# Kernel optimization log

Measured on AMD Instinct MI355X. Metric: run time of the kernel, lower is better.

## Reference

```python
import jax, jax.numpy as jnp
import numpy as np

N = 50000      # nodes
E = 1_600_000  # edges
D = 512        # input_dim == embedding_dim (see notes: fc_emb output is dead code)
H = 256        # hidden_channels
G = 16         # graphs in the batch


def setup_inputs() -> dict:
    key = jax.random.key(0)
    ks = jax.random.split(key, 16)
    x = jax.random.normal(ks[0], (N, D), dtype=jnp.float32)
    edge_index = jax.random.randint(ks[1], (2, E), 0, N, dtype=jnp.int64)
    batch = jnp.sort(jax.random.randint(ks[2], (N,), 0, G, dtype=jnp.int64))

    def lin(k, fi, fo):
        s = 1.0 / np.sqrt(fi)
        return jax.random.uniform(k, (fi, fo), jnp.float32, -s, s)

    return {
        "x": x,
        "edge_index": edge_index,
        "batch": batch,
        "W1": lin(ks[3], D, H), "b1": jnp.zeros((H,), jnp.float32),
        "W2": lin(ks[4], H, H), "b2": jnp.zeros((H,), jnp.float32),
        "W3": lin(ks[5], H, H), "b3": jnp.zeros((H,), jnp.float32),
        "Wf": lin(ks[6], H, 64), "bf": jnp.zeros((64,), jnp.float32),
        "Wp": lin(ks[7], 64, 1), "bp": jnp.zeros((1,), jnp.float32),
    }


def _gcn_conv(h, src, dst, norm, W, b):
    # GCNConv: out[i] = sum_{j->i} norm_ji * (h[j] @ W) + b  (self-loops included in src/dst)
    m = h @ W                                    # [N, out]  transform first (smaller gather)
    agg = jax.ops.segment_sum(m[src] * norm[:, None], dst, num_segments=N)
    return agg + b


def reference(x, edge_index, batch, W1, b1, W2, b2, W3, b3, Wf, bf, Wp, bp):
    loops = jnp.arange(N, dtype=edge_index.dtype)
    src = jnp.concatenate([edge_index[0], loops])   # [E+N]
    dst = jnp.concatenate([edge_index[1], loops])
    # symmetric normalization D^{-1/2} (A+I) D^{-1/2}; degree over targets incl. self-loops
    deg = jax.ops.segment_sum(jnp.ones_like(dst, jnp.float32), dst, num_segments=N)
    dinv = jnp.where(deg > 0, jax.lax.rsqrt(deg), 0.0)
    norm = dinv[src] * dinv[dst]                    # [E+N]

    h = jax.nn.relu(_gcn_conv(x, src, dst, norm, W1, b1))
    h = jax.nn.relu(_gcn_conv(h, src, dst, norm, W2, b2))
    h = _gcn_conv(h, src, dst, norm, W3, b3)

    # global_mean_pool over graph ids
    counts = jax.ops.segment_sum(jnp.ones((N,), jnp.float32), batch, num_segments=G)
    pooled = jax.ops.segment_sum(h, batch, num_segments=G) / jnp.maximum(counts, 1.0)[:, None]

    # dropout treated as identity (eval-mode determinism for baseline)
    out = pooled @ Wf + bf
    out = out @ Wp + bp
    return jax.nn.sigmoid(out)
```

## Files before the change

kernel.cpp:

```cpp
#include <hip/hip_runtime.h>
#include <hip/hip_bf16.h>

#define NN 50000
#define EE 1600000
#define DD 512
#define HH 256
#define GG 16
#define BK 96
#define NCH 256
#define CHSZ 6250

typedef long fp8x8;
typedef __attribute__((ext_vector_type(4))) float f32x4;
typedef __attribute__((ext_vector_type(2))) float f32x2;

__device__ __forceinline__ unsigned char f2fp8(float f) {
    return (unsigned char)(__builtin_amdgcn_cvt_pk_fp8_f32(f, f, 0, false) & 0xff);
}
__device__ __forceinline__ unsigned int pk4fp8(float a, float b, float c, float d) {
    unsigned int r = __builtin_amdgcn_cvt_pk_fp8_f32(a, b, 0, false);
    return __builtin_amdgcn_cvt_pk_fp8_f32(c, d, r, true);
}

__global__ __launch_bounds__(256) void k_hist_cvt(const int* __restrict__ ei,
                                                  unsigned int* __restrict__ histg,
                                                  const float* __restrict__ x, unsigned char* __restrict__ xb,
                                                  const float* __restrict__ W1, const float* __restrict__ W2,
                                                  const float* __restrict__ W3, unsigned char* __restrict__ W1t,
                                                  unsigned char* __restrict__ W2t, unsigned char* __restrict__ W3t) {
    __shared__ unsigned int hp[6250];
    int b = blockIdx.x, t = threadIdx.x;
    if (b < 1024) {
        int j = b >> 2, q = b & 3;
        int dlo = q * 12500;
        for (int i = t; i < 6250; i += 256) hp[i] = 0;
        __syncthreads();
        int base = j * CHSZ;
        for (int k = 0; k < 25; ++k) {
            int o = k * 256 + t;
            if (o < CHSZ) {
                int d = ei[EE + base + o];
                unsigned int ld = (unsigned)(d - dlo);
                if (ld < 12500u) atomicAdd(&hp[ld >> 1], (ld & 1) ? 65536u : 1u);
            }
        }
        __syncthreads();
        unsigned int* dst = histg + j * 25000 + q * 6250;
        for (int i = t; i < 6250; i += 256) dst[i] = hp[i];
    } else if (b < 7274) {
        size_t i0 = ((size_t)(b - 1024) * 256 + t) * 16;
        float4 v0 = *(const float4*)(x + i0);
        float4 v1 = *(const float4*)(x + i0 + 4);
        float4 v2 = *(const float4*)(x + i0 + 8);
        float4 v3 = *(const float4*)(x + i0 + 12);
        uint4 o;
        o.x = pk4fp8(v0.x, v0.y, v0.z, v0.w);
        o.y = pk4fp8(v1.x, v1.y, v1.z, v1.w);
        o.z = pk4fp8(v2.x, v2.y, v2.z, v2.w);
        o.w = pk4fp8(v3.x, v3.y, v3.z, v3.w);
        *(uint4*)(xb + i0) = o;
    } else {
        int u = (b - 7274) * 256 + t;
        if (u < 131072) {
            int k = u >> 8, n = u & 255;
            W1t[(size_t)n * 512 + k] = f2fp8(W1[u]);
        } else if (u < 196608) {
            int q = u - 131072; int k = q >> 8, n = q & 255;
            W2t[(size_t)n * 256 + k] = f2fp8(W2[q]);
        } else {
            int q = u - 196608; int k = q >> 8, n = q & 255;
            W3t[(size_t)n * 256 + k] = f2fp8(W3[q]);
        }
    }
}

__global__ __launch_bounds__(256) void k_scan(const unsigned int* __restrict__ histg,
                                              unsigned int* __restrict__ offg,
                                              int* __restrict__ cnt, float* __restrict__ dinv) {
    __shared__ unsigned int part[8][32];
    int t = threadIdx.x;
    int il = t & 31, g = t >> 5;
    int i = blockIdx.x * 32 + il;
    bool ok = (i < 25000);
    unsigned int hv[32];
    unsigned int p0 = 0, p1 = 0;
    if (ok) {
        const unsigned int* hp = histg + (size_t)(g * 32) * 25000 + i;
        #pragma unroll
        for (int jj = 0; jj < 32; ++jj) hv[jj] = hp[(size_t)jj * 25000];
        #pragma unroll
        for (int jj = 0; jj < 32; ++jj) { p0 += hv[jj] & 0xffffu; p1 += hv[jj] >> 16; }
    }
    part[g][il] = p0 | (p1 << 16);
    __syncthreads();
    unsigned int b0 = 0, b1 = 0;
    #pragma unroll
    for (int g2 = 0; g2 < 7; ++g2) {
        if (g2 < g) { unsigned int p = part[g2][il]; b0 += p & 0xffffu; b1 += p >> 16; }
    }
    if (ok && g == 7) {
        unsigned int tot0 = b0 + p0, tot1 = b1 + p1;
        cnt[2 * i]     = (int)tot0;
        cnt[2 * i + 1] = (int)tot1;
        dinv[2 * i]     = rsqrtf((float)tot0 + 1.0f);
        dinv[2 * i + 1] = rsqrtf((float)tot1 + 1.0f);
    }
    if (ok) {
        unsigned int run0 = b0, run1 = b1;
        unsigned int* op = offg + (size_t)(g * 32) * 25000 + i;
        #pragma unroll
        for (int jj = 0; jj < 32; ++jj) {
            op[(size_t)jj * 25000] = run0 | (run1 << 16);
            run0 += hv[jj] & 0xffffu; run1 += hv[jj] >> 16;
        }
    }
}

__global__ __launch_bounds__(256) void k_place(const int* __restrict__ ei,
                                               const unsigned int* __restrict__ offg,
                                               unsigned short* __restrict__ bucket) {
    __shared__ unsigned int cur[3125];
    int b = blockIdx.x, t = threadIdx.x;
    int x8 = b & 7, j = b >> 3;
    int lo = x8 * CHSZ;
    for (int i = t; i < 3125; i += 256) cur[i] = 0;
    __syncthreads();
    int base = j * CHSZ;
    for (int k = 0; k < 25; ++k) {
        int o = k * 256 + t;
        if (o < CHSZ) {
            int d = ei[EE + base + o];
            unsigned ld = (unsigned)(d - lo);
            if (ld < 6250u) {
                int s = ei[base + o];
                unsigned old = atomicAdd(&cur[ld >> 1], (ld & 1) ? 65536u : 1u);
                unsigned rank = (ld & 1) ? (old >> 16) : (old & 0xffffu);
                unsigned ov = offg[j * 25000 + (d >> 1)];
                unsigned pos = ((d & 1) ? (ov >> 16) : (ov & 0xffffu)) + rank;
                if (pos < BK) bucket[(size_t)d * BK + pos] = (unsigned short)s;
            }
        }
    }
}

__global__ __launch_bounds__(256) void k_gemm_fp8(const unsigned char* __restrict__ A,
                                                  const unsigned char* __restrict__ Bt,
                                                  const float* __restrict__ dinv,
                                                  unsigned char* __restrict__ C, int M, int K) {
    __shared__ unsigned char As[2][8192];
    __shared__ unsigned char Bs[2][8192];
    const int tid  = threadIdx.x;
    const int wave = tid >> 6;
    const int lane = tid & 63;
    const int row0 = blockIdx.x * 128;
    const int col0 = blockIdx.y * 128;
    const int wr = wave & 1;
    const int wc = wave >> 1;
    const int l15 = lane & 15;
    const int quad = lane >> 4;

    const int srow = (wave << 4) + (lane >> 2);
    const int gk16 = (((lane & 3) ^ (srow & 3)) << 4);
    int arow1 = row0 + srow;      if (arow1 >= M) arow1 = M - 1;
    int arow2 = row0 + srow + 64; if (arow2 >= M) arow2 = M - 1;
    const int brow1 = col0 + srow;
    const int brow2 = brow1 + 64;

#define STAGE(BUF, KB) do {                                                              \
    const unsigned char* ga1_ = A  + (size_t)arow1 * K + (KB) + gk16;                    \
    const unsigned char* ga2_ = A  + (size_t)arow2 * K + (KB) + gk16;                    \
    const unsigned char* gb1_ = Bt + (size_t)brow1 * K + (KB) + gk16;                    \
    const unsigned char* gb2_ = Bt + (size_t)brow2 * K + (KB) + gk16;                    \
    __builtin_amdgcn_global_load_lds((const __attribute__((address_space(1))) void*)ga1_,\
        (__attribute__((address_space(3))) void*)&As[BUF][wave * 1024], 16, 0, 0);       \
    __builtin_amdgcn_global_load_lds((const __attribute__((address_space(1))) void*)ga2_,\
        (__attribute__((address_space(3))) void*)&As[BUF][4096 + wave * 1024], 16, 0, 0);\
    __builtin_amdgcn_global_load_lds((const __attribute__((address_space(1))) void*)gb1_,\
        (__attribute__((address_space(3))) void*)&Bs[BUF][wave * 1024], 16, 0, 0);       \
    __builtin_amdgcn_global_load_lds((const __attribute__((address_space(1))) void*)gb2_,\
        (__attribute__((address_space(3))) void*)&Bs[BUF][4096 + wave * 1024], 16, 0, 0);\
} while (0)

    f32x4 acc[4][4];
    #pragma unroll
    for (int i = 0; i < 4; ++i)
        #pragma unroll
        for (int j = 0; j < 4; ++j)
            acc[i][j] = (f32x4){0.f, 0.f, 0.f, 0.f};

    const int NT = K >> 6;
    STAGE(0, 0);
    __syncthreads();

    for (int t = 0; t < NT; ++t) {
        const int cb = t & 1;
        if (t + 1 < NT) STAGE(cb ^ 1, (t + 1) << 6);

        fp8x8 af[2][4], bfr[2][4];
        #pragma unroll
        for (int kk = 0; kk < 2; ++kk) {
            const int csw = (((kk * 2 + (quad >> 1)) ^ (l15 & 3)) << 4) + ((quad & 1) << 3);
            #pragma unroll
            for (int mi = 0; mi < 4; ++mi) {
                af[kk][mi]  = *(const fp8x8*)&As[cb][(wr * 64 + mi * 16 + l15) * 64 + csw];
                bfr[kk][mi] = *(const fp8x8*)&Bs[cb][(wc * 64 + mi * 16 + l15) * 64 + csw];
            }
        }
        #pragma unroll
        for (int kk = 0; kk < 2; ++kk)
            #pragma unroll
            for (int mi = 0; mi < 4; ++mi)
                #pragma unroll
                for (int ni = 0; ni < 4; ++ni)
                    acc[mi][ni] = __builtin_amdgcn_mfma_f32_16x16x32_fp8_fp8(af[kk][mi], bfr[kk][ni], acc[mi][ni], 0, 0, 0);

        __syncthreads();
    }
#undef STAGE

    #pragma unroll
    for (int mi = 0; mi < 4; ++mi) {
        #pragma unroll
        for (int r = 0; r < 4; ++r) {
            int grow = row0 + wr * 64 + mi * 16 + quad * 4 + r;
            if (grow < M) {
                float ds = dinv[grow];
                #pragma unroll
                for (int ni = 0; ni < 4; ++ni) {
                    int gcol = col0 + wc * 64 + ni * 16 + l15;
                    C[(size_t)grow * 256 + gcol] = f2fp8(ds * acc[mi][ni][r]);
                }
            }
        }
    }
}

__global__ __launch_bounds__(256) void k_agg(const unsigned int* __restrict__ m,
                                             const float* __restrict__ bias,
                                             const float* __restrict__ dinv, const int* __restrict__ cnt,
                                             const unsigned short* __restrict__ bucket,
                                             unsigned int* __restrict__ outb,
                                             int do_relu) {
    int lane = threadIdx.x & 63;
    int node = blockIdx.x * 4 + (threadIdx.x >> 6);
    if (node >= NN) return;
    const unsigned int* mrow = m + lane;
    unsigned int v = mrow[(size_t)node * 64];
    f32x2 lo = __builtin_amdgcn_cvt_pk_f32_fp8(v, false);
    f32x2 hi = __builtin_amdgcn_cvt_pk_f32_fp8(v, true);
    float4 acc = make_float4(lo.x, lo.y, hi.x, hi.y);
    int n = cnt[node]; if (n > BK) n = BK;
    const unsigned short* cs = bucket + (size_t)node * BK;
    int p = 0;
    for (; p + 16 <= n; p += 16) {
        uint4 iv0 = *(const uint4*)(cs + p);
        uint4 iv1 = *(const uint4*)(cs + p + 8);
        unsigned int u0 = mrow[(size_t)(iv0.x & 0xffffu) * 64];
        unsigned int u1 = mrow[(size_t)(iv0.x >> 16)    * 64];
        unsigned int u2 = mrow[(size_t)(iv0.y & 0xffffu) * 64];
        unsigned int u3 = mrow[(size_t)(iv0.y >> 16)    * 64];
        unsigned int u4 = mrow[(size_t)(iv0.z & 0xffffu) * 64];
        unsigned int u5 = mrow[(size_t)(iv0.z >> 16)    * 64];
        unsigned int u6 = mrow[(size_t)(iv0.w & 0xffffu) * 64];
        unsigned int u7 = mrow[(size_t)(iv0.w >> 16)    * 64];
        unsigned int u8 = mrow[(size_t)(iv1.x & 0xffffu) * 64];
        unsigned int u9 = mrow[(size_t)(iv1.x >> 16)    * 64];
        unsigned int ua = mrow[(size_t)(iv1.y & 0xffffu) * 64];
        unsigned int ub = mrow[(size_t)(iv1.y >> 16)    * 64];
        unsigned int uc = mrow[(size_t)(iv1.z & 0xffffu) * 64];
        unsigned int ud = mrow[(size_t)(iv1.z >> 16)    * 64];
        unsigned int ue = mrow[(size_t)(iv1.w & 0xffffu) * 64];
        unsigned int uf = mrow[(size_t)(iv1.w >> 16)    * 64];
        f32x2 a0 = __builtin_amdgcn_cvt_pk_f32_fp8(u0, false), b0 = __builtin_amdgcn_cvt_pk_f32_fp8(u0, true);
        f32x2 a1 = __builtin_amdgcn_cvt_pk_f32_fp8(u1, false), b1 = __builtin_amdgcn_cvt_pk_f32_fp8(u1, true);
        f32x2 a2 = __builtin_amdgcn_cvt_pk_f32_fp8(u2, false), b2 = __builtin_amdgcn_cvt_pk_f32_fp8(u2, true);
        f32x2 a3 = __builtin_amdgcn_cvt_pk_f32_fp8(u3, false), b3 = __builtin_amdgcn_cvt_pk_f32_fp8(u3, true);
        f32x2 a4 = __builtin_amdgcn_cvt_pk_f32_fp8(u4, false), b4 = __builtin_amdgcn_cvt_pk_f32_fp8(u4, true);
        f32x2 a5 = __builtin_amdgcn_cvt_pk_f32_fp8(u5, false), b5 = __builtin_amdgcn_cvt_pk_f32_fp8(u5, true);
        f32x2 a6 = __builtin_amdgcn_cvt_pk_f32_fp8(u6, false), b6 = __builtin_amdgcn_cvt_pk_f32_fp8(u6, true);
        f32x2 a7 = __builtin_amdgcn_cvt_pk_f32_fp8(u7, false), b7 = __builtin_amdgcn_cvt_pk_f32_fp8(u7, true);
        f32x2 a8 = __builtin_amdgcn_cvt_pk_f32_fp8(u8, false), b8 = __builtin_amdgcn_cvt_pk_f32_fp8(u8, true);
        f32x2 a9 = __builtin_amdgcn_cvt_pk_f32_fp8(u9, false), b9 = __builtin_amdgcn_cvt_pk_f32_fp8(u9, true);
        f32x2 aa = __builtin_amdgcn_cvt_pk_f32_fp8(ua, false), ba = __builtin_amdgcn_cvt_pk_f32_fp8(ua, true);
        f32x2 ab = __builtin_amdgcn_cvt_pk_f32_fp8(ub, false), bb2 = __builtin_amdgcn_cvt_pk_f32_fp8(ub, true);
        f32x2 ac = __builtin_amdgcn_cvt_pk_f32_fp8(uc, false), bc = __builtin_amdgcn_cvt_pk_f32_fp8(uc, true);
        f32x2 ad = __builtin_amdgcn_cvt_pk_f32_fp8(ud, false), bd = __builtin_amdgcn_cvt_pk_f32_fp8(ud, true);
        f32x2 ae = __builtin_amdgcn_cvt_pk_f32_fp8(ue, false), be = __builtin_amdgcn_cvt_pk_f32_fp8(ue, true);
        f32x2 af2 = __builtin_amdgcn_cvt_pk_f32_fp8(uf, false), bf2 = __builtin_amdgcn_cvt_pk_f32_fp8(uf, true);
        acc.x += (((a0.x + a1.x) + (a2.x + a3.x)) + ((a4.x + a5.x) + (a6.x + a7.x)))
               + (((a8.x + a9.x) + (aa.x + ab.x)) + ((ac.x + ad.x) + (ae.x + af2.x)));
        acc.y += (((a0.y + a1.y) + (a2.y + a3.y)) + ((a4.y + a5.y) + (a6.y + a7.y)))
               + (((a8.y + a9.y) + (aa.y + ab.y)) + ((ac.y + ad.y) + (ae.y + af2.y)));
        acc.z += (((b0.x + b1.x) + (b2.x + b3.x)) + ((b4.x + b5.x) + (b6.x + b7.x)))
               + (((b8.x + b9.x) + (ba.x + bb2.x)) + ((bc.x + bd.x) + (be.x + bf2.x)));
        acc.w += (((b0.y + b1.y) + (b2.y + b3.y)) + ((b4.y + b5.y) + (b6.y + b7.y)))
               + (((b8.y + b9.y) + (ba.y + bb2.y)) + ((bc.y + bd.y) + (be.y + bf2.y)));
    }
    for (; p + 8 <= n; p += 8) {
        uint4 iv0 = *(const uint4*)(cs + p);
        unsigned int u0 = mrow[(size_t)(iv0.x & 0xffffu) * 64];
        unsigned int u1 = mrow[(size_t)(iv0.x >> 16)    * 64];
        unsigned int u2 = mrow[(size_t)(iv0.y & 0xffffu) * 64];
        unsigned int u3 = mrow[(size_t)(iv0.y >> 16)    * 64];
        unsigned int u4 = mrow[(size_t)(iv0.z & 0xffffu) * 64];
        unsigned int u5 = mrow[(size_t)(iv0.z >> 16)    * 64];
        unsigned int u6 = mrow[(size_t)(iv0.w & 0xffffu) * 64];
        unsigned int u7 = mrow[(size_t)(iv0.w >> 16)    * 64];
        f32x2 a0 = __builtin_amdgcn_cvt_pk_f32_fp8(u0, false), b0 = __builtin_amdgcn_cvt_pk_f32_fp8(u0, true);
        f32x2 a1 = __builtin_amdgcn_cvt_pk_f32_fp8(u1, false), b1 = __builtin_amdgcn_cvt_pk_f32_fp8(u1, true);
        f32x2 a2 = __builtin_amdgcn_cvt_pk_f32_fp8(u2, false), b2 = __builtin_amdgcn_cvt_pk_f32_fp8(u2, true);
        f32x2 a3 = __builtin_amdgcn_cvt_pk_f32_fp8(u3, false), b3 = __builtin_amdgcn_cvt_pk_f32_fp8(u3, true);
        f32x2 a4 = __builtin_amdgcn_cvt_pk_f32_fp8(u4, false), b4 = __builtin_amdgcn_cvt_pk_f32_fp8(u4, true);
        f32x2 a5 = __builtin_amdgcn_cvt_pk_f32_fp8(u5, false), b5 = __builtin_amdgcn_cvt_pk_f32_fp8(u5, true);
        f32x2 a6 = __builtin_amdgcn_cvt_pk_f32_fp8(u6, false), b6 = __builtin_amdgcn_cvt_pk_f32_fp8(u6, true);
        f32x2 a7 = __builtin_amdgcn_cvt_pk_f32_fp8(u7, false), b7 = __builtin_amdgcn_cvt_pk_f32_fp8(u7, true);
        acc.x += ((a0.x + a1.x) + (a2.x + a3.x)) + ((a4.x + a5.x) + (a6.x + a7.x));
        acc.y += ((a0.y + a1.y) + (a2.y + a3.y)) + ((a4.y + a5.y) + (a6.y + a7.y));
        acc.z += ((b0.x + b1.x) + (b2.x + b3.x)) + ((b4.x + b5.x) + (b6.x + b7.x));
        acc.w += ((b0.y + b1.y) + (b2.y + b3.y)) + ((b4.y + b5.y) + (b6.y + b7.y));
    }
    for (; p < n; ++p) {
        int s = cs[p];
        unsigned int u = mrow[(size_t)s * 64];
        f32x2 a = __builtin_amdgcn_cvt_pk_f32_fp8(u, false);
        f32x2 b = __builtin_amdgcn_cvt_pk_f32_fp8(u, true);
        acc.x += a.x; acc.y += a.y; acc.z += b.x; acc.w += b.y;
    }
    float di = dinv[node];
    const float4 bb = *(const float4*)(bias + lane * 4);
    acc.x = acc.x * di + bb.x; acc.y = acc.y * di + bb.y;
    acc.z = acc.z * di + bb.z; acc.w = acc.w * di + bb.w;
    if (do_relu) {
        acc.x = fmaxf(acc.x, 0.f); acc.y = fmaxf(acc.y, 0.f);
        acc.z = fmaxf(acc.z, 0.f); acc.w = fmaxf(acc.w, 0.f);
    }
    outb[(size_t)node * 64 + lane] = pk4fp8(acc.x, acc.y, acc.z, acc.w);
}

__global__ __launch_bounds__(256) void k_pool(const unsigned int* __restrict__ h,
                                              const int* __restrict__ batch,
                                              float* __restrict__ pooled, float* __restrict__ cnts) {
    __shared__ float pl[GG * 256];
    __shared__ float cl[GG];
    int t = threadIdx.x;
    for (int i = t; i < GG * 256; i += 256) pl[i] = 0.f;
    if (t < GG) cl[t] = 0.f;
    __syncthreads();
    int sub = t >> 6;
    int fd = t & 63;
    int chunk = (NN + gridDim.x - 1) / gridDim.x;
    int i0 = blockIdx.x * chunk;
    int i1 = i0 + chunk; if (i1 > NN) i1 = NN;
    int gcur = -1;
    float a0 = 0.f, a1 = 0.f, a2 = 0.f, a3 = 0.f, cr = 0.f;
    for (int i = i0 + sub; i < i1; i += 4) {
        int g = batch[i];
        if (g != gcur) {
            if (gcur >= 0) {
                atomicAdd(&pl[gcur * 256 + fd * 4 + 0], a0);
                atomicAdd(&pl[gcur * 256 + fd * 4 + 1], a1);
                atomicAdd(&pl[gcur * 256 + fd * 4 + 2], a2);
                atomicAdd(&pl[gcur * 256 + fd * 4 + 3], a3);
                if (fd == 0) atomicAdd(&cl[gcur], cr);
            }
            gcur = g; a0 = a1 = a2 = a3 = 0.f; cr = 0.f;
        }
        unsigned int u = h[(size_t)i * 64 + fd];
        f32x2 lo = __builtin_amdgcn_cvt_pk_f32_fp8(u, false);
        f32x2 hi = __builtin_amdgcn_cvt_pk_f32_fp8(u, true);
        a0 += lo.x; a1 += lo.y; a2 += hi.x; a3 += hi.y;
        cr += 1.f;
    }
    if (gcur >= 0) {
        atomicAdd(&pl[gcur * 256 + fd * 4 + 0], a0);
        atomicAdd(&pl[gcur * 256 + fd * 4 + 1], a1);
        atomicAdd(&pl[gcur * 256 + fd * 4 + 2], a2);
        atomicAdd(&pl[gcur * 256 + fd * 4 + 3], a3);
        if (fd == 0) atomicAdd(&cl[gcur], cr);
    }
    __syncthreads();
    for (int i = t; i < GG * 256; i += 256)
        if (pl[i] != 0.f) atomicAdd(&pooled[i], pl[i]);
    if (t < GG && cl[t] != 0.f) atomicAdd(&cnts[t], cl[t]);
}

__global__ __launch_bounds__(1024) void k_head(const float* __restrict__ pooled, const float* __restrict__ cnts,
                                               const float* __restrict__ Wf, const float* __restrict__ bf,
                                               const float* __restrict__ Wp, const float* __restrict__ bp,
                                               float* __restrict__ out) {
    __shared__ float z[GG][64];
    int t = threadIdx.x;
    int g = t >> 6, j = t & 63;
    float inv = 1.f / fmaxf(cnts[g], 1.f);
    float acc = 0.f;
    for (int k = 0; k < 256; ++k) acc += pooled[g * 256 + k] * Wf[k * 64 + j];
    z[g][j] = acc * inv + bf[j];
    __syncthreads();
    if (t < GG) {
        float o = 0.f;
        for (int j2 = 0; j2 < 64; ++j2) o += z[t][j2] * Wp[j2];
        o += bp[0];
        out[t] = 1.f / (1.f + expf(-o));
    }
}

extern "C" void kernel_launch(void* const* d_in, const int* in_sizes, int n_in,
                              void* d_out, int out_size, void* d_ws, size_t ws_size,
                              hipStream_t stream) {
    const float* x   = (const float*)d_in[0];
    const int*   ei  = (const int*)d_in[1];
    const int*   bat = (const int*)d_in[2];
    const float* W1  = (const float*)d_in[3];
    const float* b1  = (const float*)d_in[4];
    const float* W2  = (const float*)d_in[5];
    const float* b2  = (const float*)d_in[6];
    const float* W3  = (const float*)d_in[7];
    const float* b3  = (const float*)d_in[8];
    const float* Wf  = (const float*)d_in[9];
    const float* bf  = (const float*)d_in[10];
    const float* Wp  = (const float*)d_in[11];
    const float* bp  = (const float*)d_in[12];
    float* out = (float*)d_out;

    char* w = (char*)d_ws;
    unsigned char* xb  = (unsigned char*)w;  w += (size_t)NN * DD;
    unsigned char* mb  = (unsigned char*)w;  w += (size_t)NN * HH;
    unsigned char* hb  = (unsigned char*)w;  w += (size_t)NCH * 25000 * 4;
    unsigned char* hb2 = (unsigned char*)w;  w += (size_t)NCH * 25000 * 4;
    unsigned char* W1t = (unsigned char*)w;  w += (size_t)DD * HH;
    unsigned char* W2t = (unsigned char*)w;  w += (size_t)HH * HH;
    unsigned char* W3t = (unsigned char*)w;  w += (size_t)HH * HH;
    float* dinv   = (float*)w;               w += (size_t)NN * 4;
    int*   cnt    = (int*)w;                 w += (size_t)NN * 4;
    unsigned short* bucket = (unsigned short*)w; w += (size_t)NN * BK * 2;
    float* pooled = (float*)w;               w += (size_t)GG * HH * 4;
    float* cnts   = (float*)w;               w += (size_t)GG * 4;

    unsigned int* histg = (unsigned int*)hb;
    unsigned int* offg  = (unsigned int*)hb2;

    hipMemsetAsync(pooled, 0, (size_t)(GG * HH + GG) * 4, stream);

    k_hist_cvt<<<8298, 256, 0, stream>>>(ei, histg, x, xb, W1, W2, W3, W1t, W2t, W3t);
    k_scan<<<782, 256, 0, stream>>>(histg, offg, cnt, dinv);
    k_place<<<2048, 256, 0, stream>>>(ei, offg, bucket);

    dim3 gg((NN + 127) / 128, 2);
    k_gemm_fp8<<<gg, 256, 0, stream>>>(xb, W1t, dinv, mb, NN, DD);
    k_agg<<<(NN + 3) / 4, 256, 0, stream>>>((const unsigned int*)mb, b1, dinv, cnt, bucket,
                                            (unsigned int*)hb, 1);
    k_gemm_fp8<<<gg, 256, 0, stream>>>(hb, W2t, dinv, mb, NN, HH);
    k_agg<<<(NN + 3) / 4, 256, 0, stream>>>((const unsigned int*)mb, b2, dinv, cnt, bucket,
                                            (unsigned int*)hb2, 1);
    k_gemm_fp8<<<gg, 256, 0, stream>>>(hb2, W3t, dinv, mb, NN, HH);
    k_agg<<<(NN + 3) / 4, 256, 0, stream>>>((const unsigned int*)mb, b3, dinv, cnt, bucket,
                                            (unsigned int*)hb, 0);

    k_pool<<<256, 256, 0, stream>>>((const unsigned int*)hb, bat, pooled, cnts);
    k_head<<<1, 1024, 0, stream>>>(pooled, cnts, Wf, bf, Wp, bp, out);
}
```

Measured before the change: 518.5 us.

## Pack histogram to 8-bit counters, sort neighbor lists by source, fuse pool with head

Measured after the change: 545.8 us. +5.3%, slower.

```diff
diff --git a/kernel.cpp b/kernel.cpp
--- a/kernel.cpp
+++ b/kernel.cpp
@@ -30,9 +30,9 @@
                                                   unsigned char* __restrict__ W2t, unsigned char* __restrict__ W3t) {
     __shared__ unsigned int hp[6250];
     int b = blockIdx.x, t = threadIdx.x;
-    if (b < 1024) {
-        int j = b >> 2, q = b & 3;
-        int dlo = q * 12500;
+    if (b < 512) {
+        int j = b >> 1, half = b & 1;
+        int dlo = half * 25000;
         for (int i = t; i < 6250; i += 256) hp[i] = 0;
         __syncthreads();
         int base = j * CHSZ;
@@ -41,14 +41,14 @@
             if (o < CHSZ) {
                 int d = ei[EE + base + o];
                 unsigned int ld = (unsigned)(d - dlo);
-                if (ld < 12500u) atomicAdd(&hp[ld >> 1], (ld & 1) ? 65536u : 1u);
+                if (ld < 25000u) atomicAdd(&hp[ld >> 2], 1u << ((ld & 3) * 8));
             }
         }
         __syncthreads();
-        unsigned int* dst = histg + j * 25000 + q * 6250;
+        unsigned int* dst = histg + (size_t)j * 12500 + half * 6250;
         for (int i = t; i < 6250; i += 256) dst[i] = hp[i];
-    } else if (b < 7274) {
-        size_t i0 = ((size_t)(b - 1024) * 256 + t) * 16;
+    } else if (b < 6762) {
+        size_t i0 = ((size_t)(b - 512) * 256 + t) * 16;
         float4 v0 = *(const float4*)(x + i0);
         float4 v1 = *(const float4*)(x + i0 + 4);
         float4 v2 = *(const float4*)(x + i0 + 8);
@@ -60,7 +60,7 @@
         o.w = pk4fp8(v3.x, v3.y, v3.z, v3.w);
         *(uint4*)(xb + i0) = o;
     } else {
-        int u = (b - 7274) * 256 + t;
+        int u = (b - 6762) * 256 + t;
         if (u < 131072) {
             int k = u >> 8, n = u & 255;
             W1t[(size_t)n * 512 + k] = f2fp8(W1[u]);
@@ -76,42 +76,50 @@
 
 __global__ __launch_bounds__(256) void k_scan(const unsigned int* __restrict__ histg,
                                               unsigned int* __restrict__ offg,
-                                              int* __restrict__ cnt, float* __restrict__ dinv) {
-    __shared__ unsigned int part[8][32];
-    int t = threadIdx.x;
-    int il = t & 31, g = t >> 5;
-    int i = blockIdx.x * 32 + il;
-    bool ok = (i < 25000);
-    unsigned int hv[32];
-    unsigned int p0 = 0, p1 = 0;
+                                              int* __restrict__ cnt, float* __restrict__ dinv,
+                                              unsigned int* __restrict__ zero0) {
+    __shared__ unsigned int part[512];
+    int t = threadIdx.x, b = blockIdx.x;
+    if (b == 391) {
+        for (int i = t; i < GG * 256 + GG + 1; i += 256) zero0[i] = 0u;
+        return;
+    }
+    const int il = t & 31, g = t >> 5;
+    const int g4 = b * 32 + il;
+    const bool ok = (g4 < 12500);
+    unsigned hv[32];
+    unsigned s02 = 0, s13 = 0;
     if (ok) {
-        const unsigned int* hp = histg + (size_t)(g * 32) * 25000 + i;
-        #pragma unroll
-        for (int jj = 0; jj < 32; ++jj) hv[jj] = hp[(size_t)jj * 25000];
-        #pragma unroll
-        for (int jj = 0; jj < 32; ++jj) { p0 += hv[jj] & 0xffffu; p1 += hv[jj] >> 16; }
-    }
-    part[g][il] = p0 | (p1 << 16);
-    __syncthreads();
-    unsigned int b0 = 0, b1 = 0;
+        const unsigned* hp = histg + (size_t)(g * 32) * 12500 + g4;
+        #pragma unroll
+        for (int jj = 0; jj < 32; ++jj) hv[jj] = hp[(size_t)jj * 12500];
+        #pragma unroll
+        for (int jj = 0; jj < 32; ++jj) { s02 += hv[jj] & 0x00ff00ffu; s13 += (hv[jj] >> 8) & 0x00ff00ffu; }
+    }
+    part[t * 2] = s02; part[t * 2 + 1] = s13;
+    __syncthreads();
+    unsigned b02 = 0, b13 = 0;
     #pragma unroll
-    for (int g2 = 0; g2 < 7; ++g2) {
-        if (g2 < g) { unsigned int p = part[g2][il]; b0 += p & 0xffffu; b1 += p >> 16; }
-    }
+    for (int g2 = 0; g2 < 7; ++g2)
+        if (g2 < g) { b02 += part[(g2 * 32 + il) * 2]; b13 += part[(g2 * 32 + il) * 2 + 1]; }
     if (ok && g == 7) {
-        unsigned int tot0 = b0 + p0, tot1 = b1 + p1;
-        cnt[2 * i]     = (int)tot0;
-        cnt[2 * i + 1] = (int)tot1;
-        dinv[2 * i]     = rsqrtf((float)tot0 + 1.0f);
-        dinv[2 * i + 1] = rsqrtf((float)tot1 + 1.0f);
+        unsigned t02 = b02 + s02, t13 = b13 + s13;
+        int4 cv; cv.x = (int)(t02 & 0xffffu); cv.y = (int)(t13 & 0xffffu);
+        cv.z = (int)(t02 >> 16);      cv.w = (int)(t13 >> 16);
+        *(int4*)(cnt + 4 * g4) = cv;
+        float4 dv;
+        dv.x = rsqrtf((float)cv.x + 1.0f); dv.y = rsqrtf((float)cv.y + 1.0f);
+        dv.z = rsqrtf((float)cv.z + 1.0f); dv.w = rsqrtf((float)cv.w + 1.0f);
+        *(float4*)(dinv + 4 * g4) = dv;
     }
     if (ok) {
-        unsigned int run0 = b0, run1 = b1;
-        unsigned int* op = offg + (size_t)(g * 32) * 25000 + i;
+        unsigned r0 = b02 & 0xffffu, r2 = b02 >> 16, r1 = b13 & 0xffffu, r3 = b13 >> 16;
         #pragma unroll
         for (int jj = 0; jj < 32; ++jj) {
-            op[(size_t)jj * 25000] = run0 | (run1 << 16);
-            run0 += hv[jj] & 0xffffu; run1 += hv[jj] >> 16;
+            uint2 wv; wv.x = r0 | (r1 << 16); wv.y = r2 | (r3 << 16);
+            *(uint2*)(offg + (size_t)(g * 32 + jj) * 25000 + 2 * g4) = wv;
+            unsigned h = hv[jj];
+            r0 += h & 0xffu; r1 += (h >> 8) & 0xffu; r2 += (h >> 16) & 0xffu; r3 += h >> 24;
         }
     }
 }
@@ -140,6 +148,33 @@
                 if (pos < BK) bucket[(size_t)d * BK + pos] = (unsigned short)s;
             }
         }
+    }
+}
+
+__global__ __launch_bounds__(256) void k_sort(const int* __restrict__ cnt,
+                                              const unsigned short* __restrict__ bucket,
+                                              unsigned short* __restrict__ bucket2) {
+    __shared__ unsigned int binc[4][16], rk[4][16];
+    int w = threadIdx.x >> 6, l = threadIdx.x & 63;
+    int node = blockIdx.x * 4 + w;
+    if (l < 16) { binc[w][l] = 0; rk[w][l] = 0; }
+    __syncthreads();
+    int n = cnt[node]; if (n > BK) n = BK;
+    const unsigned short* cs = bucket + (size_t)node * BK;
+    unsigned s0 = 0, s1 = 0; int b0 = -1, b1 = -1;
+    if (l < n)      { s0 = cs[l];      b0 = (int)(s0 >> 12); atomicAdd(&binc[w][b0], 1u); }
+    if (l + 64 < n) { s1 = cs[l + 64]; b1 = (int)(s1 >> 12); atomicAdd(&binc[w][b1], 1u); }
+    __syncthreads();
+    unsigned short* ds = bucket2 + (size_t)node * BK;
+    if (b0 >= 0) {
+        unsigned base = 0;
+        for (int q = 0; q < b0; ++q) base += binc[w][q];
+        ds[base + atomicAdd(&rk[w][b0], 1u)] = (unsigned short)s0;
+    }
+    if (b1 >= 0) {
+        unsigned base = 0;
+        for (int q = 0; q < b1; ++q) base += binc[w][q];
+        ds[base + atomicAdd(&rk[w][b1], 1u)] = (unsigned short)s1;
     }
 }
 
@@ -337,11 +372,17 @@
     outb[(size_t)node * 64 + lane] = pk4fp8(acc.x, acc.y, acc.z, acc.w);
 }
 
-__global__ __launch_bounds__(256) void k_pool(const unsigned int* __restrict__ h,
-                                              const int* __restrict__ batch,
-                                              float* __restrict__ pooled, float* __restrict__ cnts) {
+__global__ __launch_bounds__(256) void k_poolhead(const unsigned int* __restrict__ h,
+                                                  const int* __restrict__ batch,
+                                                  float* __restrict__ pooled, float* __restrict__ cnts,
+                                                  unsigned int* __restrict__ ctr,
+                                                  const float* __restrict__ Wf, const float* __restrict__ bf,
+                                                  const float* __restrict__ Wp, const float* __restrict__ bp,
+                                                  float* __restrict__ out) {
     __shared__ float pl[GG * 256];
     __shared__ float cl[GG];
+    __shared__ float z[GG][64];
+    __shared__ unsigned int lastdone;
     int t = threadIdx.x;
     for (int i = t; i < GG * 256; i += 256) pl[i] = 0.f;
     if (t < GG) cl[t] = 0.f;
@@ -382,19 +423,25 @@
     for (int i = t; i < GG * 256; i += 256)
         if (pl[i] != 0.f) atomicAdd(&pooled[i], pl[i]);
     if (t < GG && cl[t] != 0.f) atomicAdd(&cnts[t], cl[t]);
-}
-
-__global__ __launch_bounds__(1024) void k_head(const float* __restrict__ pooled, const float* __restrict__ cnts,
-                                               const float* __restrict__ Wf, const float* __restrict__ bf,
-                                               const float* __restrict__ Wp, const float* __restrict__ bp,
-                                               float* __restrict__ out) {
-    __shared__ float z[GG][64];
-    int t = threadIdx.x;
-    int g = t >> 6, j = t & 63;
-    float inv = 1.f / fmaxf(cnts[g], 1.f);
-    float acc = 0.f;
-    for (int k = 0; k < 256; ++k) acc += pooled[g * 256 + k] * Wf[k * 64 + j];
-    z[g][j] = acc * inv + bf[j];
+
+    __syncthreads();
+    __threadfence();
+    if (t == 0) lastdone = (atomicAdd(ctr, 1u) == gridDim.x - 1) ? 1u : 0u;
+    __syncthreads();
+    if (!lastdone) return;
+    __threadfence();
+    for (int i = t; i < GG * 256; i += 256)
+        pl[i] = __hip_atomic_load(&pooled[i], __ATOMIC_RELAXED, __HIP_MEMORY_SCOPE_AGENT);
+    if (t < GG)
+        cl[t] = __hip_atomic_load(&cnts[t], __ATOMIC_RELAXED, __HIP_MEMORY_SCOPE_AGENT);
+    __syncthreads();
+    for (int idx = t; idx < GG * 64; idx += 256) {
+        int g = idx >> 6, j = idx & 63;
+        float inv = 1.f / fmaxf(cl[g], 1.f);
+        float acc = 0.f;
+        for (int k = 0; k < 256; ++k) acc += pl[g * 256 + k] * Wf[k * 64 + j];
+        z[g][j] = acc * inv + bf[j];
+    }
     __syncthreads();
     if (t < GG) {
         float o = 0.f;
@@ -432,30 +479,31 @@
     unsigned char* W3t = (unsigned char*)w;  w += (size_t)HH * HH;
     float* dinv   = (float*)w;               w += (size_t)NN * 4;
     int*   cnt    = (int*)w;                 w += (size_t)NN * 4;
-    unsigned short* bucket = (unsigned short*)w; w += (size_t)NN * BK * 2;
+    unsigned short* bucket  = (unsigned short*)w; w += (size_t)NN * BK * 2;
+    unsigned short* bucket2 = (unsigned short*)w; w += (size_t)NN * BK * 2;
     float* pooled = (float*)w;               w += (size_t)GG * HH * 4;
     float* cnts   = (float*)w;               w += (size_t)GG * 4;
+    unsigned int* ctr = (unsigned int*)w;    w += 4;
 
     unsigned int* histg = (unsigned int*)hb;
     unsigned int* offg  = (unsigned int*)hb2;
 
-    hipMemsetAsync(pooled, 0, (size_t)(GG * HH + GG) * 4, stream);
-
-    k_hist_cvt<<<8298, 256, 0, stream>>>(ei, histg, x, xb, W1, W2, W3, W1t, W2t, W3t);
-    k_scan<<<782, 256, 0, stream>>>(histg, offg, cnt, dinv);
+    k_hist_cvt<<<7786, 256, 0, stream>>>(ei, histg, x, xb, W1, W2, W3, W1t, W2t, W3t);
+    k_scan<<<392, 256, 0, stream>>>(histg, offg, cnt, dinv, (unsigned int*)pooled);
     k_place<<<2048, 256, 0, stream>>>(ei, offg, bucket);
+    k_sort<<<12500, 256, 0, stream>>>(cnt, bucket, bucket2);
 
     dim3 gg((NN + 127) / 128, 2);
     k_gemm_fp8<<<gg, 256, 0, stream>>>(xb, W1t, dinv, mb, NN, DD);
-    k_agg<<<(NN + 3) / 4, 256, 0, stream>>>((const unsigned int*)mb, b1, dinv, cnt, bucket,
+    k_agg<<<(NN + 3) / 4, 256, 0, stream>>>((const unsigned int*)mb, b1, dinv, cnt, bucket2,
                                             (unsigned int*)hb, 1);
     k_gemm_fp8<<<gg, 256, 0, stream>>>(hb, W2t, dinv, mb, NN, HH);
-    k_agg<<<(NN + 3) / 4, 256, 0, stream>>>((const unsigned int*)mb, b2, dinv, cnt, bucket,
+    k_agg<<<(NN + 3) / 4, 256, 0, stream>>>((const unsigned int*)mb, b2, dinv, cnt, bucket2,
                                             (unsigned int*)hb2, 1);
     k_gemm_fp8<<<gg, 256, 0, stream>>>(hb2, W3t, dinv, mb, NN, HH);
-    k_agg<<<(NN + 3) / 4, 256, 0, stream>>>((const unsigned int*)mb, b3, dinv, cnt, bucket,
+    k_agg<<<(NN + 3) / 4, 256, 0, stream>>>((const unsigned int*)mb, b3, dinv, cnt, bucket2,
                                             (unsigned int*)hb, 0);
 
-    k_pool<<<256, 256, 0, stream>>>((const unsigned int*)hb, bat, pooled, cnts);
-    k_head<<<1, 1024, 0, stream>>>(pooled, cnts, Wf, bf, Wp, bp, out);
-}
+    k_poolhead<<<256, 256, 0, stream>>>((const unsigned int*)hb, bat, pooled, cnts, ctr,
+                                        Wf, bf, Wp, bp, out);
+}
```
